# Kernel tuning notes

Hardware: AMD Instinct MI355X
Metric: run time of the kernel (lower is better)

## Reference

```python
import jax, jax.numpy as jnp
import numpy as np

B, N, DIM, M_DIM, FOURIER = 2, 512, 64, 16, 4
EDGE_IN = FOURIER * 2 + DIM * 2 + 1  # 137


def _mk_params(key):
    ks = jax.random.split(key, 12)
    s = 0.02
    p = {}
    p['w1e'] = jax.random.normal(ks[0], (EDGE_IN, EDGE_IN * 2), jnp.float32) * s
    p['b1e'] = jnp.zeros((EDGE_IN * 2,), jnp.float32)
    p['w2e'] = jax.random.normal(ks[1], (EDGE_IN * 2, M_DIM), jnp.float32) * s
    p['b2e'] = jnp.zeros((M_DIM,), jnp.float32)
    p['w1c'] = jax.random.normal(ks[2], (M_DIM, M_DIM * 4), jnp.float32) * s
    p['b1c'] = jnp.zeros((M_DIM * 4,), jnp.float32)
    p['w2c'] = jax.random.normal(ks[3], (M_DIM * 4, 1), jnp.float32) * s
    p['b2c'] = jnp.zeros((1,), jnp.float32)
    p['w1h'] = jax.random.normal(ks[4], (DIM + M_DIM, DIM * 2), jnp.float32) * s
    p['b1h'] = jnp.zeros((DIM * 2,), jnp.float32)
    p['w2h'] = jax.random.normal(ks[5], (DIM * 2, DIM), jnp.float32) * s
    p['b2h'] = jnp.zeros((DIM,), jnp.float32)
    return p


def setup_inputs() -> dict:
    key = jax.random.key(0)
    kf, kc, kp = jax.random.split(key, 3)
    inp = {
        'feats': jax.random.normal(kf, (B, N, DIM), jnp.float32),
        'coors': jax.random.normal(kc, (B, N, 3), jnp.float32),
    }
    inp.update(_mk_params(kp))
    return inp


def _fourier_encode_dist(x, num_encodings):
    # x: [b, i, j, 1]
    orig = x[..., None]  # [b,i,j,1,1]
    scales = 2.0 ** jnp.arange(num_encodings, dtype=x.dtype)
    xs = orig / scales  # [b,i,j,1,E]
    enc = jnp.concatenate([jnp.sin(xs), jnp.cos(xs), orig], axis=-1)  # [b,i,j,1,2E+1]
    return enc[..., 0, :]  # [b,i,j,2E+1]


def _safe_norm(rel_coors):
    sq = jnp.sum(rel_coors * rel_coors, axis=-1, keepdims=True)
    # grad-safe sqrt: torch.norm has 0 subgradient at 0
    return jnp.where(sq > 0, jnp.sqrt(jnp.where(sq > 0, sq, 1.0)), 0.0)


def _egnn_forward(feats, coors, w1e, b1e, w2e, b2e, w1c, b1c, w2c, b2c, w1h, b1h, w2h, b2h):
    b, n, d = feats.shape
    rel_coors = coors[:, :, None, :] - coors[:, None, :, :]  # [b,i,j,3]
    rel_dist = _safe_norm(rel_coors)  # [b,i,j,1]
    rel_dist = _fourier_encode_dist(rel_dist, FOURIER)  # [b,i,j,2F+1]
    feats_i = jnp.broadcast_to(feats[:, :, None, :], (b, n, n, d))
    feats_j = jnp.broadcast_to(feats[:, None, :, :], (b, n, n, d))
    edge_input = jnp.concatenate([feats_i, feats_j, rel_dist], axis=-1)  # [b,i,j,EDGE_IN]
    h = jax.nn.relu(edge_input @ w1e + b1e)
    m_ij = h @ w2e + b2e  # [b,i,j,m]
    cw = jax.nn.relu(m_ij @ w1c + b1c) @ w2c + b2c  # [b,i,j,1]
    coor_weights = cw[..., 0]  # [b,i,j]
    coors_out = jnp.einsum('bij,bijc->bic', coor_weights, rel_coors)
    m_i = jnp.sum(m_ij, axis=-2)  # [b,i,m]
    hid_in = jnp.concatenate([feats, m_i], axis=-1)
    hidden_out = jax.nn.relu(hid_in @ w1h + b1h) @ w2h + b2h
    return hidden_out, coors_out


def reference(feats, coors, w1e, b1e, w2e, b2e, w1c, b1c, w2c, b2c, w1h, b1h, w2h, b2h):
    return _egnn_forward(feats, coors, w1e, b1e, w2e, b2e, w1c, b1c, w2c, b2c, w1h, b1h, w2h, b2h)
```

## Files before the change

kernel.cpp:

```cpp
#include <hip/hip_runtime.h>
#include <math.h>
#include <stdint.h>

#define NP 288
#define OUT_H (2*512*64)

typedef _Float16 f16;
typedef __attribute__((ext_vector_type(2))) _Float16 f16x2;
typedef __attribute__((ext_vector_type(8))) _Float16 f16x8;
typedef __attribute__((ext_vector_type(4))) float f32x4;

union V8 { f16x8 v; f16x2 h[4]; };

__global__ __launch_bounds__(256) void egnn_pre(
    const float* __restrict__ feats, const float* __restrict__ w1e,
    const float* __restrict__ b1e,   const float* __restrict__ w2e,
    const float* __restrict__ w1c,
    f16* __restrict__ Q1, f16* __restrict__ P2, f16* __restrict__ Wd,
    f16* __restrict__ W2T, f16* __restrict__ W1CB)
{
    int id = blockIdx.x * 256 + threadIdx.x;
    const int NN = 1024 * NP;
    if (id < 2 * NN) {
        int hf = id / NN, r = id % NN;
        int n = r / NP, e = r % NP;
        float a = 0.f;
        if (e < 274) {
            a = hf ? 0.f : b1e[e];
            const float* fp = feats + n * 64;
            const float* wp = w1e + hf * 64 * 274 + e;
            #pragma unroll 8
            for (int d2 = 0; d2 < 64; ++d2) a += fp[d2] * wp[d2 * 274];
        }
        (hf ? P2 : Q1)[n * NP + e] = (f16)a;
    } else {
        int x = id - 2 * NN;
        if (x < 9 * NP) {
            int e = x % NP, k = x / NP;
            Wd[x] = (f16)(e < 274 ? w1e[(128 + k) * 274 + e] : 0.f);
        } else if (x < 25 * NP) {
            int y = x - 9 * NP;
            int c2 = y / NP, e = y % NP;
            W2T[y] = (f16)(e < 274 ? w2e[e * 16 + c2] : 0.f);
        } else if (x < 25 * NP + 2048) {
            int y = x - 25 * NP;
            int T = y >> 9, rem = y & 511, c2 = rem >> 5, k = rem & 31;
            W1CB[y] = (f16)(k < 16 ? w1c[k * 64 + T * 16 + c2] : 0.f);
        }
    }
}

__global__ __launch_bounds__(256) void egnn_edge(
    const float* __restrict__ feats, const float* __restrict__ coors,
    const float* __restrict__ b2e,   const float* __restrict__ b1c,
    const float* __restrict__ w2c,   const float* __restrict__ b2cv,
    const float* __restrict__ w1h,   const float* __restrict__ b1h,
    const float* __restrict__ w2h,   const float* __restrict__ b2h,
    const f16* __restrict__ Q1,  const f16* __restrict__ P2,
    const f16* __restrict__ Wd,  const f16* __restrict__ W2T,
    const f16* __restrict__ W1CB, float* __restrict__ out)
{
    __shared__ f16   sWd[9 * NP];
    __shared__ float sM[512 * 20];
    __shared__ float sHid[128];
    __shared__ float sRedM[4][16];
    __shared__ float sRedC[4][3];
    __shared__ float sFin[16];

    const int bi = blockIdx.x, bb = bi >> 9;
    const int t = threadIdx.x;
    const int lane = t & 63, wv = t >> 6;
    const int c = lane & 15, g = lane >> 4;

    {
        const uint32_t* src = (const uint32_t*)Wd;
        uint32_t* dst = (uint32_t*)sWd;
        for (int x = t; x < 9 * NP / 2; x += 256) dst[x] = src[x];
    }
    const float b2e_c = b2e[c];
    const float cix = coors[bi * 3 + 0];
    const float ciy = coors[bi * 3 + 1];
    const float ciz = coors[bi * 3 + 2];
    __syncthreads();

    const f16* Q1r = Q1 + bi * NP;
    const f16* P2b = P2 + (bb << 9) * NP;

    #pragma unroll 1
    for (int pass = 0; pass < 2; ++pass) {
        const int jbase = wv * 128 + pass * 64;

        uint32_t encPk[4][5];
        #pragma unroll
        for (int q = 0; q < 4; ++q) {
            int jg = (bb << 9) + jbase + q * 16 + c;
            float rx = cix - coors[jg * 3 + 0];
            float ry = ciy - coors[jg * 3 + 1];
            float rz = ciz - coors[jg * 3 + 2];
            float sq = rx * rx + ry * ry + rz * rz;
            float d = sq > 0.f ? sqrtf(sq) : 0.f;
            float en[9];
            #pragma unroll
            for (int k = 0; k < 4; ++k) {
                float sv, cv;
                __sincosf(d * (1.f / (float)(1 << k)), &sv, &cv);
                en[k] = sv; en[4 + k] = cv;
            }
            en[8] = d;
            #pragma unroll
            for (int p = 0; p < 4; ++p) {
                uint32_t lo = (uint32_t)__builtin_bit_cast(uint16_t, (f16)en[2 * p]);
                uint32_t hi = (uint32_t)__builtin_bit_cast(uint16_t, (f16)en[2 * p + 1]);
                encPk[q][p] = lo | (hi << 16);
            }
            encPk[q][4] = (uint32_t)__builtin_bit_cast(uint16_t, (f16)en[8]);
        }

        f32x4 acc[4] = {{0,0,0,0},{0,0,0,0},{0,0,0,0},{0,0,0,0}};

        #pragma unroll 1
        for (int s = 0; s < 9; ++s) {
            const int eo = s * 32 + g * 8;
            V8 wd[9];
            #pragma unroll
            for (int k = 0; k < 9; ++k)
                wd[k].v = *(const f16x8*)(sWd + k * NP + eo);
            f16x8 b8 = *(const f16x8*)(W2T + c * NP + eo);
            f16x8 q8 = *(const f16x8*)(Q1r + eo);

            #pragma unroll
            for (int q = 0; q < 4; ++q) {
                int j = jbase + q * 16 + c;
                V8 H;
                H.v = q8 + *(const f16x8*)(P2b + j * NP + eo);
                #pragma unroll
                for (int k = 0; k < 9; ++k) {
                    uint32_t spl = __builtin_amdgcn_perm(
                        encPk[q][k >> 1], encPk[q][k >> 1],
                        (k & 1) ? 0x07060706u : 0x05040504u);
                    f16x2 e2 = __builtin_bit_cast(f16x2, spl);
                    #pragma unroll
                    for (int p = 0; p < 4; ++p)
                        H.h[p] = __builtin_elementwise_fma(wd[k].h[p], e2, H.h[p]);
                }
                const f16x2 z2 = {(_Float16)0, (_Float16)0};
                #pragma unroll
                for (int p = 0; p < 4; ++p)
                    H.h[p] = __builtin_elementwise_max(H.h[p], z2);
                acc[q] = __builtin_amdgcn_mfma_f32_16x16x32_f16(H.v, b8, acc[q], 0, 0, 0);
            }
        }
        #pragma unroll
        for (int q = 0; q < 4; ++q) {
            int jrow = jbase + q * 16 + g * 4;
            #pragma unroll
            for (int r = 0; r < 4; ++r)
                sM[(jrow + r) * 20 + c] = acc[q][r] + b2e_c;
        }
    }
    __syncthreads();

    f16x8 aW[4];
    f32x4 b1cL[4], w2cL[4];
    #pragma unroll
    for (int T = 0; T < 4; ++T) {
        aW[T] = *(const f16x8*)(W1CB + (T * 16 + c) * 32 + g * 8);
        b1cL[T] = *(const f32x4*)(b1c + T * 16 + g * 4);
        w2cL[T] = *(const f32x4*)(w2c + T * 16 + g * 4);
    }
    const float b2c0 = b2cv[0];

    float cax = 0.f, cay = 0.f, caz = 0.f;
    float macc8[8] = {0.f,0.f,0.f,0.f,0.f,0.f,0.f,0.f};

    #pragma unroll 1
    for (int jt = 0; jt < 8; ++jt) {
        const int jrow = wv * 128 + jt * 16;
        f16x8 bm = {0,0,0,0,0,0,0,0};
        if (g < 2) {
            f32x4 m0 = *(const f32x4*)(sM + (jrow + c) * 20 + g * 8);
            f32x4 m1 = *(const f32x4*)(sM + (jrow + c) * 20 + g * 8 + 4);
            #pragma unroll
            for (int p = 0; p < 4; ++p) { macc8[p] += m0[p]; macc8[4 + p] += m1[p]; }
            bm[0]=(f16)m0[0]; bm[1]=(f16)m0[1]; bm[2]=(f16)m0[2]; bm[3]=(f16)m0[3];
            bm[4]=(f16)m1[0]; bm[5]=(f16)m1[1]; bm[6]=(f16)m1[2]; bm[7]=(f16)m1[3];
        }
        f32x4 zc = {0,0,0,0};
        float cwp = 0.f;
        #pragma unroll
        for (int T = 0; T < 4; ++T) {
            f32x4 hd = __builtin_amdgcn_mfma_f32_16x16x32_f16(aW[T], bm, zc, 0, 0, 0);
            #pragma unroll
            for (int r = 0; r < 4; ++r)
                cwp += fmaxf(hd[r] + b1cL[T][r], 0.f) * w2cL[T][r];
        }
        cwp += __shfl_xor(cwp, 16);
        cwp += __shfl_xor(cwp, 32);
        float cw = cwp + b2c0;

        int jg = (bb << 9) + jrow + c;
        float rx = cix - coors[jg * 3 + 0];
        float ry = ciy - coors[jg * 3 + 1];
        float rz = ciz - coors[jg * 3 + 2];
        cax += cw * rx; cay += cw * ry; caz += cw * rz;
    }

    #pragma unroll
    for (int msk = 1; msk <= 8; msk <<= 1)
        #pragma unroll
        for (int p = 0; p < 8; ++p) macc8[p] += __shfl_xor(macc8[p], msk);
    if (c == 0 && g < 2) {
        #pragma unroll
        for (int p = 0; p < 8; ++p) sRedM[wv][g * 8 + p] = macc8[p];
    }
    #pragma unroll
    for (int msk = 1; msk <= 32; msk <<= 1) {
        cax += __shfl_xor(cax, msk);
        cay += __shfl_xor(cay, msk);
        caz += __shfl_xor(caz, msk);
    }
    if (lane == 0) { sRedC[wv][0] = cax; sRedC[wv][1] = cay; sRedC[wv][2] = caz; }
    __syncthreads();

    if (t < 16) sFin[t] = sRedM[0][t] + sRedM[1][t] + sRedM[2][t] + sRedM[3][t];
    if (t >= 32 && t < 35) {
        int k = t - 32;
        out[OUT_H + bi * 3 + k] =
            (sRedC[0][k] + sRedC[1][k] + sRedC[2][k] + sRedC[3][k]) * 0.25f;
    }
    __syncthreads();

    if (t < 128) {
        float a = b1h[t];
        const float* fp = feats + bi * 64;
        #pragma unroll 8
        for (int k = 0; k < 64; ++k) a += fp[k] * w1h[k * 128 + t];
        #pragma unroll
        for (int k = 0; k < 16; ++k) a += sFin[k] * w1h[(64 + k) * 128 + t];
        sHid[t] = fmaxf(a, 0.f);
    }
    __syncthreads();
    if (t < 64) {
        float a = b2h[t];
        #pragma unroll 8
        for (int k = 0; k < 128; ++k) a += sHid[k] * w2h[k * 64 + t];
        out[bi * 64 + t] = a;
    }
}

extern "C" void kernel_launch(void* const* d_in, const int* in_sizes, int n_in,
                              void* d_out, int out_size, void* d_ws, size_t ws_size,
                              hipStream_t stream)
{
    const float* feats = (const float*)d_in[0];
    const float* coors = (const float*)d_in[1];
    const float* w1e   = (const float*)d_in[2];
    const float* b1e   = (const float*)d_in[3];
    const float* w2e   = (const float*)d_in[4];
    const float* b2e   = (const float*)d_in[5];
    const float* w1c   = (const float*)d_in[6];
    const float* b1c   = (const float*)d_in[7];
    const float* w2c   = (const float*)d_in[8];
    const float* b2c   = (const float*)d_in[9];
    const float* w1h   = (const float*)d_in[10];
    const float* b1h   = (const float*)d_in[11];
    const float* w2h   = (const float*)d_in[12];
    const float* b2h   = (const float*)d_in[13];
    float* out = (float*)d_out;

    char* ws = (char*)d_ws;
    f16* Q1   = (f16*)ws;
    f16* P2   = (f16*)(ws + 589824);
    f16* Wd   = (f16*)(ws + 2 * 589824);
    f16* W2T  = (f16*)(ws + 2 * 589824 + 5184);
    f16* W1CB = (f16*)(ws + 2 * 589824 + 5184 + 9216);

    egnn_pre<<<2341, 256, 0, stream>>>(feats, w1e, b1e, w2e, w1c, Q1, P2, Wd, W2T, W1CB);
    egnn_edge<<<1024, 256, 0, stream>>>(feats, coors, b2e, b1c, w2c, b2c,
                                        w1h, b1h, w2h, b2h,
                                        Q1, P2, Wd, W2T, W1CB, out);
}
```

Before: 67.39 us.

## Move edge hidden-layer Fourier/distance term onto chained 16x16x16 MFMAs

The Fourier-encoding and Q1 contributions to the first edge layer now run as a 16x16x16 f16 MFMA. A fragment-ordered copy of the Wd/Q1 weights serves as A and the per-edge encoding (plus a constant 1) as B, with the P2 slice loaded as the accumulator. ReLU is applied, the result is packed to f16 and fed straight into a second MFMA against pre-swizzled W2e fragments. This replaces many packed-f16 FMAs per edge with matrix ops. The message buffer sM is also stored as f16, which halves LDS use but costs some precision. It adds more, smaller MFMAs in a dependent chain, so latency between the two MFMAs may be exposed.

Result: slower. 78.81 us (+16.9%).

```diff
diff --git a/kernel.cpp b/kernel.cpp
--- a/kernel.cpp
+++ b/kernel.cpp
@@ -7,17 +7,37 @@
 
 typedef _Float16 f16;
 typedef __attribute__((ext_vector_type(2))) _Float16 f16x2;
+typedef __attribute__((ext_vector_type(4))) _Float16 f16x4;
 typedef __attribute__((ext_vector_type(8))) _Float16 f16x8;
 typedef __attribute__((ext_vector_type(4))) float f32x4;
 
-union V8 { f16x8 v; f16x2 h[4]; };
+static __device__ __forceinline__ f16x2 pkrtz(float a, float b) {
+    return __builtin_bit_cast(f16x2, __builtin_amdgcn_cvt_pkrtz(a, b));
+}
+
+#if defined(__has_builtin)
+#if __has_builtin(__builtin_amdgcn_mfma_f32_16x16x16f16)
+#define HAVE_MFMA16 1
+#endif
+#endif
+
+static __device__ __forceinline__ f32x4 mfma16(f16x4 a, f16x4 b, f32x4 c) {
+#ifdef HAVE_MFMA16
+    return __builtin_amdgcn_mfma_f32_16x16x16f16(a, b, c, 0, 0, 0);
+#else
+    f32x4 d;
+    asm volatile("v_mfma_f32_16x16x16_f16 %0, %1, %2, %3\n\ts_nop 7\n\ts_nop 7"
+                 : "=v"(d) : "v"(a), "v"(b), "v"(c));
+    return d;
+#endif
+}
 
 __global__ __launch_bounds__(256) void egnn_pre(
     const float* __restrict__ feats, const float* __restrict__ w1e,
     const float* __restrict__ b1e,   const float* __restrict__ w2e,
     const float* __restrict__ w1c,
     f16* __restrict__ Q1, f16* __restrict__ P2, f16* __restrict__ Wd,
-    f16* __restrict__ W2T, f16* __restrict__ W1CB)
+    f16* __restrict__ W2F, f16* __restrict__ W1CB)
 {
     int id = blockIdx.x * 256 + threadIdx.x;
     const int NN = 1024 * NP;
@@ -38,12 +58,18 @@
         if (x < 9 * NP) {
             int e = x % NP, k = x / NP;
             Wd[x] = (f16)(e < 274 ? w1e[(128 + k) * 274 + e] : 0.f);
-        } else if (x < 25 * NP) {
+        } else if (x < 9 * NP + 1152) {
             int y = x - 9 * NP;
-            int c2 = y / NP, e = y % NP;
-            W2T[y] = (f16)(e < 274 ? w2e[e * 16 + c2] : 0.f);
-        } else if (x < 25 * NP + 2048) {
-            int y = x - 25 * NP;
+            int S = y >> 6, l = y & 63, cc = l & 15, gg = l >> 4;
+            f16x4 v = {0, 0, 0, 0};
+            #pragma unroll
+            for (int jj = 0; jj < 4; ++jj) {
+                int e = S * 16 + gg * 4 + jj;
+                v[jj] = (f16)(e < 274 ? w2e[e * 16 + cc] : 0.f);
+            }
+            *(f16x4*)(W2F + y * 4) = v;
+        } else if (x < 9 * NP + 1152 + 2048) {
+            int y = x - 9 * NP - 1152;
             int T = y >> 9, rem = y & 511, c2 = rem >> 5, k = rem & 31;
             W1CB[y] = (f16)(k < 16 ? w1c[k * 64 + T * 16 + c2] : 0.f);
         }
@@ -57,11 +83,12 @@
     const float* __restrict__ w1h,   const float* __restrict__ b1h,
     const float* __restrict__ w2h,   const float* __restrict__ b2h,
     const f16* __restrict__ Q1,  const f16* __restrict__ P2,
-    const f16* __restrict__ Wd,  const f16* __restrict__ W2T,
+    const f16* __restrict__ Wd,  const f16* __restrict__ W2F,
     const f16* __restrict__ W1CB, float* __restrict__ out)
 {
-    __shared__ f16   sWd[9 * NP];
-    __shared__ float sM[512 * 20];
+    __shared__ f16x4 sA1f[1152];
+    __shared__ f16x4 sB2f[1152];
+    __shared__ __align__(16) f16 sM[512 * 16];
     __shared__ float sHid[128];
     __shared__ float sRedM[4][16];
     __shared__ float sRedC[4][3];
@@ -73,9 +100,19 @@
     const int c = lane & 15, g = lane >> 4;
 
     {
-        const uint32_t* src = (const uint32_t*)Wd;
-        uint32_t* dst = (uint32_t*)sWd;
-        for (int x = t; x < 9 * NP / 2; x += 256) dst[x] = src[x];
+        const uint2* src = (const uint2*)W2F;
+        uint2* dst = (uint2*)sB2f;
+        for (int x = t; x < 1152; x += 256) dst[x] = src[x];
+        const f16* Q1r = Q1 + bi * NP;
+        for (int x = t; x < 1152; x += 256) {
+            int S = x >> 6, l = x & 63, cc = l & 15, gg = l >> 4;
+            int e = S * 16 + cc;
+            f16x4 v = {0, 0, 0, 0};
+            if (gg == 0)      { v[0]=Wd[0*NP+e]; v[1]=Wd[1*NP+e]; v[2]=Wd[2*NP+e]; v[3]=Wd[3*NP+e]; }
+            else if (gg == 1) { v[0]=Wd[4*NP+e]; v[1]=Wd[5*NP+e]; v[2]=Wd[6*NP+e]; v[3]=Wd[7*NP+e]; }
+            else if (gg == 2) { v[0]=Wd[8*NP+e]; v[1]=Q1r[e]; }
+            sA1f[x] = v;
+        }
     }
     const float b2e_c = b2e[c];
     const float cix = coors[bi * 3 + 0];
@@ -83,79 +120,52 @@
     const float ciz = coors[bi * 3 + 2];
     __syncthreads();
 
-    const f16* Q1r = Q1 + bi * NP;
     const f16* P2b = P2 + (bb << 9) * NP;
 
     #pragma unroll 1
     for (int pass = 0; pass < 2; ++pass) {
         const int jbase = wv * 128 + pass * 64;
-
-        uint32_t encPk[4][5];
-        #pragma unroll
-        for (int q = 0; q < 4; ++q) {
-            int jg = (bb << 9) + jbase + q * 16 + c;
+        #pragma unroll 1
+        for (int J4 = 0; J4 < 4; ++J4) {
+            const int j = jbase + J4 * 16 + c;
+            const int jg = (bb << 9) + j;
             float rx = cix - coors[jg * 3 + 0];
             float ry = ciy - coors[jg * 3 + 1];
             float rz = ciz - coors[jg * 3 + 2];
             float sq = rx * rx + ry * ry + rz * rz;
             float d = sq > 0.f ? sqrtf(sq) : 0.f;
-            float en[9];
-            #pragma unroll
-            for (int k = 0; k < 4; ++k) {
-                float sv, cv;
-                __sincosf(d * (1.f / (float)(1 << k)), &sv, &cv);
-                en[k] = sv; en[4 + k] = cv;
+            float en[8];
+            #pragma unroll
+            for (int k = 0; k < 4; ++k)
+                __sincosf(d * (1.f / (float)(1 << k)), &en[k], &en[4 + k]);
+            f16x2 p01 = pkrtz(en[0], en[1]);
+            f16x2 p23 = pkrtz(en[2], en[3]);
+            f16x2 p45 = pkrtz(en[4], en[5]);
+            f16x2 p67 = pkrtz(en[6], en[7]);
+            f16x2 pd1 = pkrtz(d, 1.0f);
+            f16x2 zz = {(_Float16)0, (_Float16)0};
+            f16x2 lo = (g == 0) ? p01 : (g == 1) ? p45 : (g == 2) ? pd1 : zz;
+            f16x2 hi = (g == 0) ? p23 : (g == 1) ? p67 : zz;
+            f16x4 b1 = __builtin_shufflevector(lo, hi, 0, 1, 2, 3);
+
+            const f16* cp = P2b + j * NP + g * 4;
+            f32x4 acc = {0.f, 0.f, 0.f, 0.f};
+            #pragma unroll
+            for (int S = 0; S < 18; ++S) {
+                f16x4 a1 = sA1f[S * 64 + lane];
+                f16x4 b2 = sB2f[S * 64 + lane];
+                f16x4 c4 = *(const f16x4*)(cp + S * 16);
+                f32x4 cf = {(float)c4[0], (float)c4[1], (float)c4[2], (float)c4[3]};
+                f32x4 h = mfma16(a1, b1, cf);
+                f16x2 hA = pkrtz(fmaxf(h[0], 0.f), fmaxf(h[1], 0.f));
+                f16x2 hB = pkrtz(fmaxf(h[2], 0.f), fmaxf(h[3], 0.f));
+                f16x4 a2 = __builtin_shufflevector(hA, hB, 0, 1, 2, 3);
+                acc = mfma16(a2, b2, acc);
             }
-            en[8] = d;
-            #pragma unroll
-            for (int p = 0; p < 4; ++p) {
-                uint32_t lo = (uint32_t)__builtin_bit_cast(uint16_t, (f16)en[2 * p]);
-                uint32_t hi = (uint32_t)__builtin_bit_cast(uint16_t, (f16)en[2 * p + 1]);
-                encPk[q][p] = lo | (hi << 16);
-            }
-            encPk[q][4] = (uint32_t)__builtin_bit_cast(uint16_t, (f16)en[8]);
-        }
-
-        f32x4 acc[4] = {{0,0,0,0},{0,0,0,0},{0,0,0,0},{0,0,0,0}};
-
-        #pragma unroll 1
-        for (int s = 0; s < 9; ++s) {
-            const int eo = s * 32 + g * 8;
-            V8 wd[9];
-            #pragma unroll
-            for (int k = 0; k < 9; ++k)
-                wd[k].v = *(const f16x8*)(sWd + k * NP + eo);
-            f16x8 b8 = *(const f16x8*)(W2T + c * NP + eo);
-            f16x8 q8 = *(const f16x8*)(Q1r + eo);
-
-            #pragma unroll
-            for (int q = 0; q < 4; ++q) {
-                int j = jbase + q * 16 + c;
-                V8 H;
-                H.v = q8 + *(const f16x8*)(P2b + j * NP + eo);
-                #pragma unroll
-                for (int k = 0; k < 9; ++k) {
-                    uint32_t spl = __builtin_amdgcn_perm(
-                        encPk[q][k >> 1], encPk[q][k >> 1],
-                        (k & 1) ? 0x07060706u : 0x05040504u);
-                    f16x2 e2 = __builtin_bit_cast(f16x2, spl);
-                    #pragma unroll
-                    for (int p = 0; p < 4; ++p)
-                        H.h[p] = __builtin_elementwise_fma(wd[k].h[p], e2, H.h[p]);
-                }
-                const f16x2 z2 = {(_Float16)0, (_Float16)0};
-                #pragma unroll
-                for (int p = 0; p < 4; ++p)
-                    H.h[p] = __builtin_elementwise_max(H.h[p], z2);
-                acc[q] = __builtin_amdgcn_mfma_f32_16x16x32_f16(H.v, b8, acc[q], 0, 0, 0);
-            }
-        }
-        #pragma unroll
-        for (int q = 0; q < 4; ++q) {
-            int jrow = jbase + q * 16 + g * 4;
+            const int jr = jbase + J4 * 16 + g * 4;
             #pragma unroll
             for (int r = 0; r < 4; ++r)
-                sM[(jrow + r) * 20 + c] = acc[q][r] + b2e_c;
+                sM[(jr + r) * 16 + c] = (f16)(acc[r] + b2e_c);
         }
     }
     __syncthreads();
@@ -178,12 +188,9 @@
         const int jrow = wv * 128 + jt * 16;
         f16x8 bm = {0,0,0,0,0,0,0,0};
         if (g < 2) {
-            f32x4 m0 = *(const f32x4*)(sM + (jrow + c) * 20 + g * 8);
-            f32x4 m1 = *(const f32x4*)(sM + (jrow + c) * 20 + g * 8 + 4);
-            #pragma unroll
-            for (int p = 0; p < 4; ++p) { macc8[p] += m0[p]; macc8[4 + p] += m1[p]; }
-            bm[0]=(f16)m0[0]; bm[1]=(f16)m0[1]; bm[2]=(f16)m0[2]; bm[3]=(f16)m0[3];
-            bm[4]=(f16)m1[0]; bm[5]=(f16)m1[1]; bm[6]=(f16)m1[2]; bm[7]=(f16)m1[3];
+            bm = *(const f16x8*)(sM + (jrow + c) * 16 + g * 8);
+            #pragma unroll
+            for (int p = 0; p < 8; ++p) macc8[p] += (float)bm[p];
         }
         f32x4 zc = {0,0,0,0};
         float cwp = 0.f;
@@ -271,12 +278,12 @@
     char* ws = (char*)d_ws;
     f16* Q1   = (f16*)ws;
     f16* P2   = (f16*)(ws + 589824);
-    f16* Wd   = (f16*)(ws + 2 * 589824);
-    f16* W2T  = (f16*)(ws + 2 * 589824 + 5184);
-    f16* W1CB = (f16*)(ws + 2 * 589824 + 5184 + 9216);
-
-    egnn_pre<<<2341, 256, 0, stream>>>(feats, w1e, b1e, w2e, w1c, Q1, P2, Wd, W2T, W1CB);
+    f16* Wd   = (f16*)(ws + 1179648);
+    f16* W2F  = (f16*)(ws + 1179648 + 5184);
+    f16* W1CB = (f16*)(ws + 1179648 + 5184 + 9216);
+
+    egnn_pre<<<2327, 256, 0, stream>>>(feats, w1e, b1e, w2e, w1c, Q1, P2, Wd, W2F, W1CB);
     egnn_edge<<<1024, 256, 0, stream>>>(feats, coors, b2e, b1c, w2c, b2c,
                                         w1h, b1h, w2h, b2h,
-                                        Q1, P2, Wd, W2T, W1CB, out);
-}
+                                        Q1, P2, Wd, W2F, W1CB, out);
+}
```
